# Kernel tuning notes

Hardware: AMD Instinct MI355X
Metric: run time of the kernel (lower is better)

## Reference

```python
import jax, jax.numpy as jnp
import numpy as np

B, N, F_IN, S, F_OUT = 16, 128, 8, 8, 64
KN_HID = 32  # kernel_network=[32]
FC_HID = 32


def setup_inputs() -> dict:
    key = jax.random.key(0)
    ks = jax.random.split(key, 13)
    # sparse-ish binary adjacency (batch mode, dense storage)
    A = (jax.random.uniform(ks[0], (B, N, N)) < 0.1).astype(jnp.float32)
    X = jax.random.normal(ks[1], (B, N, F_IN), jnp.float32)
    E = jax.random.normal(ks[2], (B, N, N, S), jnp.float32)
    sc = 0.1
    return {
        "A": A, "X": X, "E": E,
        # ECCConv edge-kernel network: Dense(32, relu) -> Dense(F_IN*F_OUT, linear)
        "kn_w1": jax.random.normal(ks[3], (S, KN_HID), jnp.float32) * sc,
        "kn_b1": jnp.zeros((KN_HID,), jnp.float32),
        "kn_w2": jax.random.normal(ks[4], (KN_HID, F_IN * F_OUT), jnp.float32) * sc,
        "kn_b2": jnp.zeros((F_IN * F_OUT,), jnp.float32),
        # ECCConv root weight + bias
        "root_w": jax.random.normal(ks[5], (F_IN, F_OUT), jnp.float32) * sc,
        "conv_b": jnp.zeros((F_OUT,), jnp.float32),
        # Dense(32, relu)
        "fc_w": jax.random.normal(ks[6], (F_OUT, FC_HID), jnp.float32) * sc,
        "fc_b": jnp.zeros((FC_HID,), jnp.float32),
        # Dense(1, sigmoid)
        "out_w": jax.random.normal(ks[7], (FC_HID, 1), jnp.float32) * sc,
        "out_b": jnp.zeros((1,), jnp.float32),
    }


def reference(A, X, E, kn_w1, kn_b1, kn_w2, kn_b2, root_w, conv_b,
              fc_w, fc_b, out_w, out_b):
    # --- ECCConv (Spektral, batch mode) ---
    # edge-conditioned kernel network: per edge-pair MLP
    h = jax.nn.relu(E @ kn_w1 + kn_b1)            # [B,N,N,32]
    kernel = h @ kn_w2 + kn_b2                    # [B,N,N,F_in*F_out]
    kernel = kernel.reshape(A.shape[0], A.shape[1], A.shape[2], X.shape[-1], root_w.shape[-1])
    kernel = kernel * A[..., None, None]          # mask by adjacency
    # out[b,n,o] = sum_{i,f} kernel[b,n,i,f,o] * X[b,i,f]
    out = jnp.einsum("bnifo,bif->bno", kernel, X)
    out = out + X @ root_w + conv_b               # root weight + bias
    x = jax.nn.relu(out)                          # [B,N,F_out]
    # --- GlobalAvgPool over nodes ---
    x = x.mean(axis=1)                            # [B,F_out]
    # --- Dense head ---
    x = jax.nn.relu(x @ fc_w + fc_b)              # [B,32]
    return jax.nn.sigmoid(x @ out_w + out_b)      # [B,1]
```

## Files before the change

kernel.cpp:

```cpp
#include <hip/hip_runtime.h>
#include <math.h>

#define B_    16
#define N_    128
#define F_IN_ 8
#define S_    8
#define F_OUT_ 64
#define KN_HID_ 32
#define FC_HID_ 32

#define NODE_OFF  0

__device__ __forceinline__ int next_edge(unsigned long long& lo,
                                         unsigned long long& hi) {
    if (lo) { int i = __builtin_ctzll(lo); lo &= lo - 1; return i; }
    if (hi) { int i = __builtin_ctzll(hi) + 64; hi &= hi - 1; return i; }
    return -1;
}

__global__ __launch_bounds__(256) void k2_fused(
    const float* __restrict__ A, const float* __restrict__ X,
    const float* __restrict__ E,
    const float* __restrict__ kn_w1, const float* __restrict__ kn_b1,
    const float* __restrict__ kn_w2, const float* __restrict__ kn_b2,
    const float* __restrict__ root_w, const float* __restrict__ conv_b,
    float* __restrict__ ws)
{
    __shared__ float Xlds[N_ * F_IN_];
    __shared__ float Elds[4][N_ * S_];
    __shared__ float Tlds[4][264];

    const int t    = threadIdx.x;
    const int lane = t & 63;
    const int wave = t >> 6;
    const int h2   = lane >> 5;
    const int j    = lane & 31;
    const int b    = blockIdx.x >> 5;
    const int bn   = blockIdx.x * 4 + wave;

    ((float4*)Xlds)[t] = ((const float4*)(X + b * N_ * F_IN_))[t];

    {
        const float4* __restrict__ src = (const float4*)(E + (size_t)bn * N_ * S_);
        float4* __restrict__ dst = (float4*)Elds[wave];
#pragma unroll
        for (int r = 0; r < 4; ++r)
            dst[lane + 64 * r] = src[lane + 64 * r];
    }

    float w1j[S_];
#pragma unroll
    for (int s = 0; s < S_; ++s) w1j[s] = kn_w1[s * KN_HID_ + j];
    const float b1j = kn_b1[j];

    const float a0 = A[(size_t)bn * N_ + lane];
    const float a1 = A[(size_t)bn * N_ + 64 + lane];
    unsigned long long mlo = __ballot(a0 != 0.f);
    unsigned long long mhi = __ballot(a1 != 0.f);

    __syncthreads();

    const float4* __restrict__ Xl4 = (const float4*)Xlds;
    const float4* __restrict__ El4 = (const float4*)Elds[wave];

    float T[4]  = {0.f, 0.f, 0.f, 0.f};
    float xs[4] = {0.f, 0.f, 0.f, 0.f};

    int i0 = next_edge(mlo, mhi);
    float4 eA0, eA1;
    if (i0 >= 0) { eA0 = El4[i0 * 2]; eA1 = El4[i0 * 2 + 1]; }
    int i1 = (i0 >= 0) ? next_edge(mlo, mhi) : -1;
    float4 eB0, eB1;
    if (i1 >= 0) { eB0 = El4[i1 * 2]; eB1 = El4[i1 * 2 + 1]; }

    while (i0 >= 0) {
        const int i2 = (i1 >= 0) ? next_edge(mlo, mhi) : -1;
        float4 eC0, eC1;
        if (i2 >= 0) { eC0 = El4[i2 * 2]; eC1 = El4[i2 * 2 + 1]; }

        const float ha = fmaf(eA0.x, w1j[0], fmaf(eA0.y, w1j[1],
                         fmaf(eA0.z, w1j[2], eA0.w * w1j[3])));
        const float hb = fmaf(eA1.x, w1j[4], fmaf(eA1.y, w1j[5],
                         fmaf(eA1.z, w1j[6], eA1.w * w1j[7])));
        float hv = b1j + ha + hb;
        hv = hv > 0.f ? hv : 0.f;

        const float4 xf = Xl4[i0 * 2 + h2];
        T[0] = fmaf(hv, xf.x, T[0]);  T[1] = fmaf(hv, xf.y, T[1]);
        T[2] = fmaf(hv, xf.z, T[2]);  T[3] = fmaf(hv, xf.w, T[3]);
        xs[0] += xf.x; xs[1] += xf.y; xs[2] += xf.z; xs[3] += xf.w;

        i0 = i1; eA0 = eB0; eA1 = eB1;
        i1 = i2; eB0 = eC0; eB1 = eC1;
    }

    float4* __restrict__ Tl4 = (float4*)Tlds[wave];
    Tl4[j * 2 + h2] = make_float4(T[0], T[1], T[2], T[3]);
    if (j == 0)
        Tl4[64 + h2] = make_float4(xs[0], xs[1], xs[2], xs[3]);

    const int q = lane & 15;
    const int g = lane >> 4;
    const float* __restrict__ T0 = Tlds[wave];
    const float4* __restrict__ W4 = (const float4*)kn_w2;
    const float4* __restrict__ B4 = (const float4*)kn_b2;

    float4 acc = make_float4(0.f, 0.f, 0.f, 0.f);
#pragma unroll 8
    for (int kf = g; kf < 256; kf += 4) {
        const float4 w = W4[kf * 16 + q];
        const float t0 = T0[kf];
        acc.x += t0 * w.x; acc.y += t0 * w.y; acc.z += t0 * w.z; acc.w += t0 * w.w;
    }
#pragma unroll
    for (int f = g; f < F_IN_; f += 4) {
        const float4 w = B4[f * 16 + q];
        const float t0 = T0[256 + f];
        acc.x += t0 * w.x; acc.y += t0 * w.y; acc.z += t0 * w.z; acc.w += t0 * w.w;
    }

#pragma unroll
    for (int d = 16; d < 64; d <<= 1) {
        acc.x += __shfl_xor(acc.x, d); acc.y += __shfl_xor(acc.y, d);
        acc.z += __shfl_xor(acc.z, d); acc.w += __shfl_xor(acc.w, d);
    }

    const float4* __restrict__ R4 = (const float4*)root_w;
    const float4 cb = ((const float4*)conv_b)[q];
    const int n = bn & (N_ - 1);
    float4 r = acc;
    r.x += cb.x; r.y += cb.y; r.z += cb.z; r.w += cb.w;
#pragma unroll
    for (int f = 0; f < F_IN_; ++f) {
        const float xv = Xlds[n * F_IN_ + f];
        const float4 rw = R4[f * 16 + q];
        r.x += xv * rw.x; r.y += xv * rw.y; r.z += xv * rw.z; r.w += xv * rw.w;
    }
    r.x = r.x > 0.f ? r.x : 0.f;  r.y = r.y > 0.f ? r.y : 0.f;
    r.z = r.z > 0.f ? r.z : 0.f;  r.w = r.w > 0.f ? r.w : 0.f;
    if (g == 0)
        ((float4*)(ws + NODE_OFF + (size_t)bn * F_OUT_))[q] = r;
}

__global__ __launch_bounds__(256) void k3_head(
    const float* __restrict__ fc_w, const float* __restrict__ fc_b,
    const float* __restrict__ out_w, const float* __restrict__ out_b,
    const float* __restrict__ ws, float* __restrict__ out)
{
    const int b = blockIdx.x;
    const int t = threadIdx.x;
    const int o = t & 63;
    const int g = t >> 6;

    float p = 0.f;
    for (int n = g; n < N_; n += 4)
        p += ws[NODE_OFF + (size_t)(b * N_ + n) * F_OUT_ + o];

    __shared__ float red[4][F_OUT_];
    __shared__ float pm[F_OUT_];
    __shared__ float y[FC_HID_];
    red[g][o] = p;
    __syncthreads();

    if (t < F_OUT_)
        pm[t] = (red[0][t] + red[1][t] + red[2][t] + red[3][t]) * (1.0f / (float)N_);
    __syncthreads();

    if (t < FC_HID_) {
        float v = fc_b[t];
#pragma unroll
        for (int o2 = 0; o2 < F_OUT_; ++o2) v += pm[o2] * fc_w[o2 * FC_HID_ + t];
        y[t] = v > 0.f ? v : 0.f;
    }
    __syncthreads();

    if (t == 0) {
        float z = out_b[0];
#pragma unroll
        for (int qq = 0; qq < FC_HID_; ++qq) z += y[qq] * out_w[qq];
        out[b] = 1.f / (1.f + expf(-z));
    }
}

extern "C" void kernel_launch(void* const* d_in, const int* in_sizes, int n_in,
                              void* d_out, int out_size, void* d_ws, size_t ws_size,
                              hipStream_t stream)
{
    const float* A      = (const float*)d_in[0];
    const float* X      = (const float*)d_in[1];
    const float* E      = (const float*)d_in[2];
    const float* kn_w1  = (const float*)d_in[3];
    const float* kn_b1  = (const float*)d_in[4];
    const float* kn_w2  = (const float*)d_in[5];
    const float* kn_b2  = (const float*)d_in[6];
    const float* root_w = (const float*)d_in[7];
    const float* conv_b = (const float*)d_in[8];
    const float* fc_w   = (const float*)d_in[9];
    const float* fc_b   = (const float*)d_in[10];
    const float* out_w  = (const float*)d_in[11];
    const float* out_b  = (const float*)d_in[12];

    float* ws  = (float*)d_ws;
    float* out = (float*)d_out;

    k2_fused<<<B_ * N_ / 4, 256, 0, stream>>>(A, X, E, kn_w1, kn_b1,
                                              kn_w2, kn_b2, root_w, conv_b, ws);
    k3_head<<<B_, 256, 0, stream>>>(fc_w, fc_b, out_w, out_b, ws, out);
}
```

Baseline: 100.9 us.

## Share kn_w2 loads across eight nodes per block and pre-pool node outputs

Blocks now cover eight nodes with 512 threads. The kernel-network second-layer projection is split by K-slice across waves, so each kn_w2 float4 is loaded once and applied to all eight nodes' T vectors from LDS, then reduced across waves through shared memory. The block also sums its eight node outputs before writing, so the head kernel reads 16 partial sums per graph instead of 128 rows. The cost is more LDS use, extra block barriers and eight accumulator float4s per thread, which may lower occupancy.

```diff
diff --git a/kernel.cpp b/kernel.cpp
--- a/kernel.cpp
+++ b/kernel.cpp
@@ -18,7 +18,7 @@
     return -1;
 }
 
-__global__ __launch_bounds__(256) void k2_fused(
+__global__ __launch_bounds__(512) void k2_fused(
     const float* __restrict__ A, const float* __restrict__ X,
     const float* __restrict__ E,
     const float* __restrict__ kn_w1, const float* __restrict__ kn_b1,
@@ -27,18 +27,20 @@
     float* __restrict__ ws)
 {
     __shared__ float Xlds[N_ * F_IN_];
-    __shared__ float Elds[4][N_ * S_];
-    __shared__ float Tlds[4][264];
+    __shared__ float Elds[8][N_ * S_];
+    __shared__ float Tlds[8][264];
+    __shared__ float Red[8][8][F_OUT_];
+    __shared__ float Pool[8][F_OUT_];
 
     const int t    = threadIdx.x;
     const int lane = t & 63;
     const int wave = t >> 6;
     const int h2   = lane >> 5;
     const int j    = lane & 31;
-    const int b    = blockIdx.x >> 5;
-    const int bn   = blockIdx.x * 4 + wave;
-
-    ((float4*)Xlds)[t] = ((const float4*)(X + b * N_ * F_IN_))[t];
+    const int b    = blockIdx.x >> 4;
+    const int bn   = blockIdx.x * 8 + wave;
+
+    ((float2*)Xlds)[t] = ((const float2*)(X + b * N_ * F_IN_))[t];
 
     {
         const float4* __restrict__ src = (const float4*)(E + (size_t)bn * N_ * S_);
@@ -99,47 +101,90 @@
     if (j == 0)
         Tl4[64 + h2] = make_float4(xs[0], xs[1], xs[2], xs[3]);
 
+    __syncthreads();
+
     const int q = lane & 15;
     const int g = lane >> 4;
-    const float* __restrict__ T0 = Tlds[wave];
     const float4* __restrict__ W4 = (const float4*)kn_w2;
     const float4* __restrict__ B4 = (const float4*)kn_b2;
-
-    float4 acc = make_float4(0.f, 0.f, 0.f, 0.f);
-#pragma unroll 8
-    for (int kf = g; kf < 256; kf += 4) {
+    const int base = wave * 32;
+
+    float4 acc[8];
+#pragma unroll
+    for (int nd = 0; nd < 8; ++nd) acc[nd] = make_float4(0.f, 0.f, 0.f, 0.f);
+
+#pragma unroll
+    for (int kf2 = g; kf2 < 32; kf2 += 4) {
+        const int kf = base + kf2;
         const float4 w = W4[kf * 16 + q];
-        const float t0 = T0[kf];
-        acc.x += t0 * w.x; acc.y += t0 * w.y; acc.z += t0 * w.z; acc.w += t0 * w.w;
-    }
-#pragma unroll
-    for (int f = g; f < F_IN_; f += 4) {
-        const float4 w = B4[f * 16 + q];
-        const float t0 = T0[256 + f];
-        acc.x += t0 * w.x; acc.y += t0 * w.y; acc.z += t0 * w.z; acc.w += t0 * w.w;
+#pragma unroll
+        for (int nd = 0; nd < 8; ++nd) {
+            const float tv = Tlds[nd][kf];
+            acc[nd].x = fmaf(tv, w.x, acc[nd].x);
+            acc[nd].y = fmaf(tv, w.y, acc[nd].y);
+            acc[nd].z = fmaf(tv, w.z, acc[nd].z);
+            acc[nd].w = fmaf(tv, w.w, acc[nd].w);
+        }
+    }
+    if (g == 0) {
+        const float4 w = B4[wave * 16 + q];
+#pragma unroll
+        for (int nd = 0; nd < 8; ++nd) {
+            const float tv = Tlds[nd][256 + wave];
+            acc[nd].x = fmaf(tv, w.x, acc[nd].x);
+            acc[nd].y = fmaf(tv, w.y, acc[nd].y);
+            acc[nd].z = fmaf(tv, w.z, acc[nd].z);
+            acc[nd].w = fmaf(tv, w.w, acc[nd].w);
+        }
     }
 
 #pragma unroll
     for (int d = 16; d < 64; d <<= 1) {
-        acc.x += __shfl_xor(acc.x, d); acc.y += __shfl_xor(acc.y, d);
-        acc.z += __shfl_xor(acc.z, d); acc.w += __shfl_xor(acc.w, d);
-    }
-
-    const float4* __restrict__ R4 = (const float4*)root_w;
-    const float4 cb = ((const float4*)conv_b)[q];
-    const int n = bn & (N_ - 1);
-    float4 r = acc;
-    r.x += cb.x; r.y += cb.y; r.z += cb.z; r.w += cb.w;
-#pragma unroll
-    for (int f = 0; f < F_IN_; ++f) {
-        const float xv = Xlds[n * F_IN_ + f];
-        const float4 rw = R4[f * 16 + q];
-        r.x += xv * rw.x; r.y += xv * rw.y; r.z += xv * rw.z; r.w += xv * rw.w;
-    }
-    r.x = r.x > 0.f ? r.x : 0.f;  r.y = r.y > 0.f ? r.y : 0.f;
-    r.z = r.z > 0.f ? r.z : 0.f;  r.w = r.w > 0.f ? r.w : 0.f;
-    if (g == 0)
-        ((float4*)(ws + NODE_OFF + (size_t)bn * F_OUT_))[q] = r;
+#pragma unroll
+        for (int nd = 0; nd < 8; ++nd) {
+            acc[nd].x += __shfl_xor(acc[nd].x, d);
+            acc[nd].y += __shfl_xor(acc[nd].y, d);
+            acc[nd].z += __shfl_xor(acc[nd].z, d);
+            acc[nd].w += __shfl_xor(acc[nd].w, d);
+        }
+    }
+
+    if (g == 0) {
+#pragma unroll
+        for (int nd = 0; nd < 8; ++nd)
+            ((float4*)Red[wave][nd])[q] = acc[nd];
+    }
+    __syncthreads();
+
+    if (g == 0) {
+        const float4 cb = ((const float4*)conv_b)[q];
+        float4 r = cb;
+#pragma unroll
+        for (int pw = 0; pw < 8; ++pw) {
+            const float4 p = ((const float4*)Red[pw][wave])[q];
+            r.x += p.x; r.y += p.y; r.z += p.z; r.w += p.w;
+        }
+        const int n = bn & (N_ - 1);
+        const float4* __restrict__ R4 = (const float4*)root_w;
+#pragma unroll
+        for (int f = 0; f < F_IN_; ++f) {
+            const float xv = Xlds[n * F_IN_ + f];
+            const float4 rw = R4[f * 16 + q];
+            r.x = fmaf(xv, rw.x, r.x); r.y = fmaf(xv, rw.y, r.y);
+            r.z = fmaf(xv, rw.z, r.z); r.w = fmaf(xv, rw.w, r.w);
+        }
+        r.x = r.x > 0.f ? r.x : 0.f;  r.y = r.y > 0.f ? r.y : 0.f;
+        r.z = r.z > 0.f ? r.z : 0.f;  r.w = r.w > 0.f ? r.w : 0.f;
+        ((float4*)Pool[wave])[q] = r;
+    }
+    __syncthreads();
+
+    if (wave == 0) {
+        float s = 0.f;
+#pragma unroll
+        for (int nd = 0; nd < 8; ++nd) s += Pool[nd][lane];
+        ws[NODE_OFF + (size_t)blockIdx.x * F_OUT_ + lane] = s;
+    }
 }
 
 __global__ __launch_bounds__(256) void k3_head(
@@ -153,8 +198,8 @@
     const int g = t >> 6;
 
     float p = 0.f;
-    for (int n = g; n < N_; n += 4)
-        p += ws[NODE_OFF + (size_t)(b * N_ + n) * F_OUT_ + o];
+    for (int s = g; s < 16; s += 4)
+        p += ws[NODE_OFF + (size_t)(b * 16 + s) * F_OUT_ + o];
 
     __shared__ float red[4][F_OUT_];
     __shared__ float pm[F_OUT_];
@@ -203,7 +248,7 @@
     float* ws  = (float*)d_ws;
     float* out = (float*)d_out;
 
-    k2_fused<<<B_ * N_ / 4, 256, 0, stream>>>(A, X, E, kn_w1, kn_b1,
+    k2_fused<<<B_ * N_ / 8, 512, 0, stream>>>(A, X, E, kn_w1, kn_b1,
                                               kn_w2, kn_b2, root_w, conv_b, ws);
     k3_head<<<B_, 256, 0, stream>>>(fc_w, fc_b, out_w, out_b, ws, out);
 }
```

Measured after the change: 96.08 us, median of 2. -4.8%, faster.
